# Optimization experiments

Measured on AMD Instinct MI355X. Metric: run time of the kernel, lower is better.

Reference implementation:

```python
import jax, jax.numpy as jnp
import numpy as np

BN_INV = 1.0 / np.float32(np.sqrt(1.0 + 1e-5))  # eval BN with running_mean=0, running_var=1


def _conv(x, w, stride):
    return jax.lax.conv_general_dilated(
        x, w, (stride, stride), [(1, 1), (1, 1)],
        dimension_numbers=('NCHW', 'OIHW', 'NCHW'))


def _se(x, w1, b1, w2, b2):
    # squeeze-excite: global avg pool -> fc -> relu -> fc -> sigmoid -> scale
    y = x.mean(axis=(2, 3))                       # (B, C)
    y = jax.nn.relu(y @ w1.T + b1)
    y = jax.nn.sigmoid(y @ w2.T + b2)
    return x * y[:, :, None, None]


def _squash(s):
    n2 = jnp.sum(s * s, axis=-1, keepdims=True)
    n = jnp.sqrt(n2)
    return s * (n2 / (1.0 + n2)) / (n + 1e-8)


def _block(x, cw, g, b, s1w, s1b, s2w, s2b, stride):
    h = _conv(x, cw, stride)
    h = h * (g * BN_INV)[None, :, None, None] + b[None, :, None, None]
    h = jax.nn.relu(h)
    return _se(h, s1w, s1b, s2w, s2b)


def setup_inputs() -> dict:
    key = jax.random.key(0)
    ks = jax.random.split(key, 32)
    rn = lambda i, shape, s=1.0: s * jax.random.normal(ks[i], shape, dtype=jnp.float32)
    d = {}
    d['x'] = rn(0, (64, 1, 128, 128))
    # feature extractor
    d['conv1_w'] = rn(1, (16, 1, 3, 3), 0.3)
    d['bn1_g'] = 1.0 + rn(2, (16,), 0.1)
    d['bn1_b'] = rn(3, (16,), 0.1)
    d['se1_w1'] = rn(4, (1, 16), 0.2); d['se1_b1'] = rn(5, (1,), 0.1)
    d['se1_w2'] = rn(6, (16, 1), 0.2); d['se1_b2'] = rn(7, (16,), 0.1)
    d['conv2_w'] = rn(8, (32, 16, 3, 3), 0.1)
    d['bn2_g'] = 1.0 + rn(9, (32,), 0.1)
    d['bn2_b'] = rn(10, (32,), 0.1)
    d['se2_w1'] = rn(11, (2, 32), 0.2); d['se2_b1'] = rn(12, (2,), 0.1)
    d['se2_w2'] = rn(13, (32, 2), 0.2); d['se2_b2'] = rn(14, (32,), 0.1)
    d['conv3_w'] = rn(15, (64, 32, 3, 3), 0.07)
    d['bn3_g'] = 1.0 + rn(16, (64,), 0.1)
    d['bn3_b'] = rn(17, (64,), 0.1)
    d['se3_w1'] = rn(18, (4, 64), 0.15); d['se3_b1'] = rn(19, (4,), 0.1)
    d['se3_w2'] = rn(20, (64, 4), 0.15); d['se3_b2'] = rn(21, (64,), 0.1)
    # primary capsules conv: 64 -> 8 caps * 8 dim = 64 channels, stride 2
    d['pc_w'] = rn(22, (64, 64, 3, 3), 0.05)
    d['pc_b'] = rn(23, (64,), 0.05)
    # digit capsule transform: (1, 2048, 3, 16, 8)
    d['W_digit'] = 0.01 * jax.random.normal(ks[24], (1, 2048, 3, 16, 8), dtype=jnp.float32)
    return d


def reference(x, conv1_w, bn1_g, bn1_b, se1_w1, se1_b1, se1_w2, se1_b2,
              conv2_w, bn2_g, bn2_b, se2_w1, se2_b1, se2_w2, se2_b2,
              conv3_w, bn3_g, bn3_b, se3_w1, se3_b1, se3_w2, se3_b2,
              pc_w, pc_b, W_digit):
    h = _block(x, conv1_w, bn1_g, bn1_b, se1_w1, se1_b1, se1_w2, se1_b2, 1)
    h = _block(h, conv2_w, bn2_g, bn2_b, se2_w1, se2_b1, se2_w2, se2_b2, 2)
    h = _block(h, conv3_w, bn3_g, bn3_b, se3_w1, se3_b1, se3_w2, se3_b2, 2)
    # primary capsules: conv -> (B, 8 caps, 8 dim, 16*16) -> (B, 2048, 8)
    u = _conv(h, pc_w, 2) + pc_b[None, :, None, None]     # (B, 64, 16, 16)
    B = u.shape[0]
    u = u.reshape(B, 8, 8, -1).transpose(0, 1, 3, 2).reshape(B, -1, 8)
    u = _squash(u)                                        # (B, 2048, 8)
    # u_hat[b,i,c,d] = sum_e W[0,i,c,d,e] * u[b,i,e]  (avoids torch's W.repeat)
    u_hat = jnp.einsum('icde,bie->bicd', W_digit[0], u)   # (B, 2048, 3, 16)
    b_ij = jnp.zeros((B, u_hat.shape[1], u_hat.shape[2], 1), u_hat.dtype)
    v_j = None
    for _ in range(3):  # fixed routing iterations
        c_ij = jax.nn.softmax(b_ij, axis=2)
        s_j = jnp.sum(c_ij * u_hat, axis=1, keepdims=True)  # (B,1,3,16)
        v_j = _squash(s_j)
        b_ij = b_ij + jnp.sum(u_hat * v_j, axis=-1, keepdims=True)
    v = v_j[:, 0]                                          # (B, 3, 16)
    return jnp.sqrt(jnp.sum(v * v, axis=-1))               # (B, 3) class lengths
```

## Files before the change

kernel.cpp:

```cpp
#include <hip/hip_runtime.h>
#include <math.h>

#define BN_INV_F 0.9999950000374997f

__device__ __forceinline__ void gload_lds4(const float* g, float* l) {
    __builtin_amdgcn_global_load_lds(
        (const __attribute__((address_space(1))) void*)g,
        (__attribute__((address_space(3))) void*)l, 4, 0, 0);
}
__device__ __forceinline__ void gload_lds16(const float* g, float* l) {
    __builtin_amdgcn_global_load_lds(
        (const __attribute__((address_space(1))) void*)g,
        (__attribute__((address_space(3))) void*)l, 16, 0, 0);
}

__global__ __launch_bounds__(256) void wtrans_all_k(
    const float* __restrict__ w1, const float* __restrict__ w2,
    const float* __restrict__ w3, const float* __restrict__ wp,
    float* __restrict__ w1t, float* __restrict__ w2t,
    float* __restrict__ w3t, float* __restrict__ wpt)
{
    int i = blockIdx.x * 256 + threadIdx.x;
    if (i < 144) {
        int co = i % 16, k = i / 16;
        w1t[i] = w1[co * 9 + k];
    } else if (i < 4752) {
        int t = i - 144;
        int co = t % 32, rk = t / 32, cin = rk / 9, k = rk % 9;
        w2t[t] = w2[(co * 16 + cin) * 9 + k];
    } else if (i < 23184) {
        int t = i - 4752;
        int co = t % 64, rk = t / 64, cin = rk / 9, k = rk % 9;
        w3t[t] = w3[(co * 32 + cin) * 9 + k];
    } else if (i < 60048) {
        int t = i - 23184;
        int co = t % 64, rk = t / 64, cin = rk / 9, k = rk % 9;
        wpt[t] = wp[(co * 64 + cin) * 9 + k];
    }
}

template <int CIN, int CINB, int COUT, int COB, int HIN, int HOUT, int STRIDE,
          int TW, int ROWS_T, int PPT, int CB, int NTHREADS,
          bool BN_RELU, bool SE_SUM, int HSE_IN, int KSPLIT>
__device__ __forceinline__ void conv_body(
    const float* __restrict__ in, const float* __restrict__ wt,
    const float* __restrict__ gamma, const float* __restrict__ beta,
    float* __restrict__ out, size_t pstride,
    float* __restrict__ se_sum, const float* __restrict__ se_sums_in,
    const float* __restrict__ se_w1, const float* __restrict__ se_b1,
    const float* __restrict__ se_w2, const float* __restrict__ se_b2,
    float inv_spatial)
{
    constexpr int WIN = HIN, WOUT = HOUT;
    constexpr int TH = ROWS_T * PPT;
    constexpr int IH_T = (TH - 1) * STRIDE + 3;
    constexpr int NW = NTHREADS / 64;
    constexpr int NCHUNK = CINB / CB;
    constexpr int SEGS = (WIN >= 64) ? (WIN / 64) : 1;
    constexpr int PAIRS = (IH_T + 1) / 2;
    constexpr int NG = COUT / COB;
    constexpr int IHW = IH_T * WIN;
    constexpr int CHUNK_BYTES = CB * IHW * 4;
    constexpr bool FAST16 = (CHUNK_BYTES % 1024) == 0;
    constexpr int NISS = CHUNK_BYTES / 1024;
    static_assert(NTHREADS == TW * ROWS_T, "geometry");
    static_assert(TW == WOUT, "tile must span full output width");
    static_assert(CINB % CB == 0, "chunking");
    static_assert(WIN % 64 == 0 || WIN == 32, "stage width");

    const int b = blockIdx.z;
    const int gy = blockIdx.y;
    const int ty = blockIdx.x;
    const int tid = threadIdx.x;
    const int wo = tid % TW;
    const int rg = tid / TW;
    const int g = gy % NG;
    const int kk = gy / NG;
    const int cin0 = kk * CINB;

    __shared__ float in_t[2][CB * IH_T * WIN];
    __shared__ float scl[CIN];
    __shared__ float gl[COB], bl[COB];
    __shared__ float red[NW][COB];
    __shared__ float hid[HSE_IN > 0 ? HSE_IN : 1];

    const float* inb = in + (size_t)b * CIN * HIN * WIN;
    const int gr0 = ty * TH * STRIDE - 1;
    const int wos = wo * STRIDE;
    const int wvid = tid >> 6, lane = tid & 63;
    const bool interior = (gr0 >= 0) && (gr0 + IH_T <= HIN);

    auto stage = [&](int c, int buf) {
        const int cb0 = cin0 + c * CB;
        float* bb = &in_t[buf][0];
        if (FAST16 && interior) {
            for (int i = wvid; i < NISS; i += NW) {
                int fe = i * 256 + lane * 4;
                int ci = fe / IHW;
                int rem = fe - ci * IHW;
                int lr = rem / WIN;
                int lc = rem - lr * WIN;
                const float* gsrc = inb + (size_t)(cb0 + ci) * (HIN * WIN)
                                  + (size_t)(gr0 + lr) * WIN + lc;
                gload_lds16(gsrc, bb + i * 256);
            }
        } else if (WIN >= 64) {
            for (int r = wvid; r < CB * IH_T; r += NW) {
                int ci = r / IH_T, lr = r - ci * IH_T;
                int gr = gr0 + lr;
                float* ldst = bb + (ci * IH_T + lr) * WIN;
                if (gr >= 0 && gr < HIN) {
                    const float* gsrc = inb + (size_t)(cb0 + ci) * HIN * WIN + (size_t)gr * WIN;
#pragma unroll
                    for (int s = 0; s < SEGS; ++s)
                        gload_lds4(gsrc + s * 64 + lane, ldst + s * 64);
                } else {
#pragma unroll
                    for (int s = 0; s < SEGS; ++s) ldst[s * 64 + lane] = 0.0f;
                }
            }
        } else {
            for (int pz = wvid; pz < CB * PAIRS; pz += NW) {
                int ci = pz / PAIRS, q = pz - ci * PAIRS;
                int lr0 = q * 2;
                int nr = (lr0 + 1 < IH_T) ? 2 : 1;
                int grr = gr0 + lr0;
                float* ldst = bb + (ci * IH_T + lr0) * WIN;
                if (nr == 2 && grr >= 0 && grr + 1 < HIN) {
                    const float* gsrc = inb + (size_t)(cb0 + ci) * HIN * WIN + (size_t)grr * WIN + lane;
                    gload_lds4(gsrc, ldst);
                } else {
                    for (int e = lane; e < nr * WIN; e += 64) {
                        int rr = e / WIN, cc = e - rr * WIN;
                        int gr = grr + rr;
                        ldst[e] = (gr >= 0 && gr < HIN)
                            ? inb[(size_t)(cb0 + ci) * HIN * WIN + (size_t)gr * WIN + cc] : 0.0f;
                    }
                }
            }
        }
    };

    stage(0, 0);

    if (HSE_IN > 0) {
        if (tid < HSE_IN) {
            float a = se_b1[tid];
            for (int c = 0; c < CIN; ++c)
                a = fmaf(se_sums_in[b * CIN + c] * inv_spatial, se_w1[tid * CIN + c], a);
            hid[tid] = fmaxf(a, 0.0f);
        }
        __syncthreads();
        if (tid < CIN) {
            float a = se_b2[tid];
            for (int h = 0; h < HSE_IN; ++h)
                a = fmaf(hid[h], se_w2[tid * HSE_IN + h], a);
            scl[tid] = 1.0f / (1.0f + expf(-a));
        }
    } else {
        for (int t = tid; t < CIN; t += NTHREADS) scl[t] = 1.0f;
    }
    if (tid < COB) {
        int co = g * COB + tid;
        if (BN_RELU) {
            gl[tid] = gamma[co] * BN_INV_F;
            bl[tid] = beta[co];
        } else {
            gl[tid] = (kk == 0) ? gamma[co] : 0.0f;
        }
    }

    float acc[PPT][COB];
#pragma unroll
    for (int p = 0; p < PPT; ++p)
#pragma unroll
        for (int co = 0; co < COB; ++co) acc[p][co] = 0.0f;

    int cur = 0;
    for (int c = 0; c < NCHUNK; ++c) {
        asm volatile("s_waitcnt vmcnt(0)" ::: "memory");
        __syncthreads();
        if (c + 1 < NCHUNK) stage(c + 1, cur ^ 1);

        const float* bb = &in_t[cur][0];
#pragma unroll
        for (int ci = 0; ci < CB; ++ci) {
            const int cw = cin0 + c * CB + ci;
            const float sc = scl[cw];
            const float* wtap = wt + (size_t)cw * 9 * COUT + g * COB;
            const float* bb_ci = bb + ci * IH_T * WIN;
#pragma unroll
            for (int kh = 0; kh < 3; ++kh) {
#pragma unroll
                for (int kw = 0; kw < 3; ++kw) {
                    const float* wrow = wtap + (kh * 3 + kw) * COUT;
#pragma unroll
                    for (int p = 0; p < PPT; ++p) {
                        const float* row = bb_ci + ((rg + p * ROWS_T) * STRIDE + kh) * WIN;
                        int wi = wos + kw - 1;
                        float v;
                        if (kw == 0) {
                            v = row[wi < 0 ? 0 : wi];
                            if (wi < 0) v = 0.0f;
                        } else if (STRIDE == 1 && kw == 2) {
                            v = row[wi >= WIN ? WIN - 1 : wi];
                            if (wi >= WIN) v = 0.0f;
                        } else {
                            v = row[wi];
                        }
                        v *= sc;
#pragma unroll
                        for (int co = 0; co < COB; ++co)
                            acc[p][co] = fmaf(wrow[co], v, acc[p][co]);
                    }
                }
            }
        }
        cur ^= 1;
    }

    float tsum[COB];
#pragma unroll
    for (int co = 0; co < COB; ++co) tsum[co] = 0.0f;
    float* ob = out + (size_t)kk * pstride
              + ((size_t)b * COUT + (size_t)g * COB) * HOUT * WOUT;
#pragma unroll
    for (int p = 0; p < PPT; ++p) {
        const int ho = ty * TH + rg + p * ROWS_T;
#pragma unroll
        for (int co = 0; co < COB; ++co) {
            float v;
            if (BN_RELU)
                v = fmaxf(fmaf(acc[p][co], gl[co], bl[co]), 0.0f);
            else
                v = acc[p][co] + gl[co];
            ob[(size_t)co * HOUT * WOUT + ho * WOUT + wo] = v;
            tsum[co] += v;
        }
    }

    if (SE_SUM) {
#pragma unroll
        for (int co = 0; co < COB; ++co) {
            float v = tsum[co];
            for (int off = 32; off; off >>= 1) v += __shfl_down(v, off, 64);
            if (lane == 0) red[wvid][co] = v;
        }
        __syncthreads();
        if (tid < COB) {
            float v = 0.0f;
#pragma unroll
            for (int k = 0; k < NW; ++k) v += red[k][tid];
            atomicAdd(&se_sum[b * COUT + g * COB + tid], v);
        }
    }
}

template <int CIN, int CINB, int COUT, int WCO, int HIN, int HOUT, int STRIDE,
          int TW, int PPT, int CB, int NTHREADS,
          bool BN_RELU, bool SE_SUM, int HSE_IN, int KSPLIT>
__device__ __forceinline__ void conv_ws_body(
    const float* __restrict__ in, const float* __restrict__ wt,
    const float* __restrict__ gamma, const float* __restrict__ beta,
    float* __restrict__ out, size_t pstride,
    float* __restrict__ se_sum, const float* __restrict__ se_sums_in,
    const float* __restrict__ se_w1, const float* __restrict__ se_b1,
    const float* __restrict__ se_w2, const float* __restrict__ se_b2,
    float inv_spatial)
{
    constexpr int WIN = HIN, WOUT = HOUT;
    constexpr int NW = NTHREADS / 64;
    constexpr int WROWS = 64 / TW;
    constexpr int TH = WROWS * PPT;
    constexpr int IH_T = (TH - 1) * STRIDE + 3;
    constexpr int COBT = NW * WCO;
    constexpr int NG = COUT / COBT;
    constexpr int NCHUNK = CINB / CB;
    constexpr int SEGS = WIN / 64;
    constexpr int HALF = WIN / 2;
    static_assert(STRIDE == 2, "wave-split body is stride-2 only");
    static_assert(TW == WOUT, "tile spans full width");
    static_assert(CINB % CB == 0, "chunking");
    static_assert(WIN % 64 == 0, "stage width");
    static_assert(COUT % COBT == 0, "cout split");

    const int b = blockIdx.z;
    const int gy = blockIdx.y;
    const int ty = blockIdx.x;
    const int tid = threadIdx.x;
    const int lane = tid & 63;
    const int wvu = __builtin_amdgcn_readfirstlane(tid >> 6);
    const int wo = lane % TW;
    const int rl = lane / TW;
    const int g = gy % NG;
    const int kk = gy / NG;
    const int cin0 = kk * CINB;

    __shared__ float in_t[2][CB * IH_T * WIN];
    __shared__ float scl[CIN];
    __shared__ float gl[COBT], bl[COBT];
    __shared__ float red[NW][WCO];
    __shared__ float hid[HSE_IN > 0 ? HSE_IN : 1];

    const float* inb = in + (size_t)b * CIN * HIN * WIN;
    const int gr0 = ty * TH * STRIDE - 1;

    auto stage = [&](int c, int buf) {
        const int cb0 = cin0 + c * CB;
        float* bb = &in_t[buf][0];
        for (int r = wvu; r < CB * IH_T; r += NW) {
            int ci = r / IH_T, lr = r - ci * IH_T;
            int gr = gr0 + lr;
            float* ldst = bb + (ci * IH_T + lr) * WIN;
            if (gr >= 0 && gr < HIN) {
                const float* gsrc = inb + (size_t)(cb0 + ci) * HIN * WIN + (size_t)gr * WIN;
#pragma unroll
                for (int s = 0; s < SEGS; ++s) {
                    int p = s * 64 + lane;
                    int half = p / HALF;
                    int idx = p - half * HALF;
                    gload_lds4(gsrc + 2 * idx + half, ldst + s * 64);
                }
            } else {
#pragma unroll
                for (int s = 0; s < SEGS; ++s) ldst[s * 64 + lane] = 0.0f;
            }
        }
    };

    stage(0, 0);

    if (HSE_IN > 0) {
        if (tid < HSE_IN) {
            float a = se_b1[tid];
            for (int c = 0; c < CIN; ++c)
                a = fmaf(se_sums_in[b * CIN + c] * inv_spatial, se_w1[tid * CIN + c], a);
            hid[tid] = fmaxf(a, 0.0f);
        }
        __syncthreads();
        if (tid < CIN) {
            float a = se_b2[tid];
            for (int h = 0; h < HSE_IN; ++h)
                a = fmaf(hid[h], se_w2[tid * HSE_IN + h], a);
            scl[tid] = 1.0f / (1.0f + expf(-a));
        }
    } else {
        for (int t = tid; t < CIN; t += NTHREADS) scl[t] = 1.0f;
    }
    if (tid < COBT) {
        int co = g * COBT + tid;
        if (BN_RELU) {
            gl[tid] = gamma[co] * BN_INV_F;
            bl[tid] = beta[co];
        } else {
            gl[tid] = (kk == 0) ? gamma[co] : 0.0f;
        }
    }

    float acc[PPT][WCO];
#pragma unroll
    for (int p = 0; p < PPT; ++p)
#pragma unroll
        for (int co = 0; co < WCO; ++co) acc[p][co] = 0.0f;

    int cur = 0;
    for (int c = 0; c < NCHUNK; ++c) {
        asm volatile("s_waitcnt vmcnt(0)" ::: "memory");
        __syncthreads();
        if (c + 1 < NCHUNK) stage(c + 1, cur ^ 1);

        const float* bb = &in_t[cur][0];
#pragma unroll
        for (int ci = 0; ci < CB; ++ci) {
            const int cw = cin0 + c * CB + ci;
            const float sc = scl[cw];
            const float* wtap = wt + (size_t)cw * 9 * COUT + g * COBT + wvu * WCO;
            const float* bb_ci = bb + ci * IH_T * WIN;
#pragma unroll
            for (int kh = 0; kh < 3; ++kh) {
                float iwv[PPT][3];
#pragma unroll
                for (int p = 0; p < PPT; ++p) {
                    const float* row = bb_ci + ((rl + p * WROWS) * STRIDE + kh) * WIN;
                    float e  = row[wo];
                    float om = row[HALF + ((wo == 0) ? 0 : wo - 1)];
                    if (wo == 0) om = 0.0f;
                    float op = row[HALF + wo];
                    iwv[p][0] = om * sc;
                    iwv[p][1] = e * sc;
                    iwv[p][2] = op * sc;
                }
#pragma unroll
                for (int kw = 0; kw < 3; ++kw) {
                    const float* wrow = wtap + (kh * 3 + kw) * COUT;
#pragma unroll
                    for (int p = 0; p < PPT; ++p) {
                        const float v = iwv[p][kw];
#pragma unroll
                        for (int co = 0; co < WCO; ++co)
                            acc[p][co] = fmaf(wrow[co], v, acc[p][co]);
                    }
                }
            }
        }
        cur ^= 1;
    }

    float tsum[WCO];
#pragma unroll
    for (int co = 0; co < WCO; ++co) tsum[co] = 0.0f;
    float* ob = out + (size_t)kk * pstride
              + ((size_t)b * COUT + (size_t)g * COBT + (size_t)wvu * WCO) * HOUT * WOUT;
#pragma unroll
    for (int p = 0; p < PPT; ++p) {
        const int ho = ty * TH + rl + p * WROWS;
#pragma unroll
        for (int co = 0; co < WCO; ++co) {
            float v;
            if (BN_RELU)
                v = fmaxf(fmaf(acc[p][co], gl[wvu * WCO + co], bl[wvu * WCO + co]), 0.0f);
            else
                v = acc[p][co] + gl[wvu * WCO + co];
            ob[(size_t)co * HOUT * WOUT + ho * WOUT + wo] = v;
            tsum[co] += v;
        }
    }

    if (SE_SUM) {
#pragma unroll
        for (int co = 0; co < WCO; ++co) {
            float v = tsum[co];
            for (int off = 32; off; off >>= 1) v += __shfl_down(v, off, 64);
            if (lane == 0) red[wvu][co] = v;
        }
        __syncthreads();
        if (lane < WCO)
            atomicAdd(&se_sum[b * COUT + g * COBT + wvu * WCO + lane], red[wvu][lane]);
    }
}

#define CONV_ARGS \
    const float* __restrict__ in, const float* __restrict__ wt, \
    const float* __restrict__ gamma, const float* __restrict__ beta, \
    float* __restrict__ out, size_t pstride, float* __restrict__ se_sum, \
    const float* __restrict__ se_sums_in, \
    const float* __restrict__ se_w1, const float* __restrict__ se_b1, \
    const float* __restrict__ se_w2, const float* __restrict__ se_b2, \
    float inv_spatial
#define CONV_PASS in, wt, gamma, beta, out, pstride, se_sum, se_sums_in, \
    se_w1, se_b1, se_w2, se_b2, inv_spatial

__global__ __launch_bounds__(256) void conv1_k(CONV_ARGS) {
    conv_body<1, 1, 16, 16, 128, 128, 1, 128, 2, 2, 1, 256, true, true, 0, 1>(CONV_PASS);
}
__global__ __launch_bounds__(256) void conv2_k(CONV_ARGS) {
    conv_ws_body<16, 16, 32, 8, 128, 64, 2, 64, 2, 4, 256, true, true, 1, 1>(CONV_PASS);
}
__global__ __launch_bounds__(512) void conv3_k(CONV_ARGS) {
    conv_ws_body<32, 32, 64, 8, 64, 32, 2, 32, 1, 8, 512, true, true, 2, 1>(CONV_PASS);
}
__global__ __launch_bounds__(256) void pc_k(CONV_ARGS) {
    conv_body<64, 16, 64, 16, 32, 16, 2, 16, 16, 1, 4, 256, false, false, 4, 4>(CONV_PASS);
}

__global__ __launch_bounds__(256) void squash_uhat_k(
    const float* __restrict__ up, size_t pstride,
    const float* __restrict__ W, float* __restrict__ u_hat)
{
    const int base = blockIdx.x * 256;
    const int tid = threadIdx.x;
    __shared__ float ush[256][8];

    {
        const int cap = base + tid;
        const int b = cap >> 11, i = cap & 2047;
        const int chi = i >> 8, spx = i & 255;
        const size_t off = ((size_t)(b * 64 + chi * 8)) * 256 + spx;
        float s[8];
        float n2 = 0.0f;
#pragma unroll
        for (int j = 0; j < 8; j++) {
            const size_t o = off + (size_t)j * 256;
            s[j] = (up[o] + up[o + pstride]) + (up[o + 2 * pstride] + up[o + 3 * pstride]);
            n2 = fmaf(s[j], s[j], n2);
        }
        const float n = sqrtf(n2);
        const float f = (n2 / (1.0f + n2)) / (n + 1e-8f);
#pragma unroll
        for (int j = 0; j < 8; j++) ush[tid][j] = s[j] * f;
    }
    __syncthreads();

    float* ob = u_hat + (size_t)base * 48;
#pragma unroll 4
    for (int k = 0; k < 48; ++k) {
        int o = tid + k * 256;
        int c = o / 48, cd = o % 48;
        int gi = (base + c) & 2047;
        const float* wp = W + (size_t)gi * 384 + cd * 8;
        float a = 0.0f;
#pragma unroll
        for (int e = 0; e < 8; e++) a = fmaf(wp[e], ush[c][e], a);
        ob[o] = a;
    }
}

template <int IT>
__global__ __launch_bounds__(256) void sweep_k(const float* __restrict__ u_hat,
                                               const float* __restrict__ s_hist,
                                               float* __restrict__ s_out)
{
    const int b = blockIdx.y;
    const int i = blockIdx.x * 256 + threadIdx.x;
    const int tid = threadIdx.x;
    __shared__ float vsh[IT > 0 ? IT : 1][48];
    __shared__ float fac[IT > 0 ? IT : 1][3];
    __shared__ float red[4][48];

    const float4* qp = (const float4*)(u_hat + ((size_t)b * 2048 + i) * 48);
    float uhv[48];
#pragma unroll
    for (int q = 0; q < 12; ++q) {
        float4 t = qp[q];
        uhv[q * 4 + 0] = t.x; uhv[q * 4 + 1] = t.y;
        uhv[q * 4 + 2] = t.z; uhv[q * 4 + 3] = t.w;
    }

    if (IT > 0) {
        if (tid < IT * 48) {
            int t = tid / 48, c = tid % 48;
            vsh[t][c] = s_hist[((size_t)t * 64 + b) * 48 + c];
        }
        __syncthreads();
        if (tid < IT * 3) {
            int t = tid / 3, j = tid % 3;
            float n2 = 0.0f;
            for (int d = 0; d < 16; ++d) { float s = vsh[t][j * 16 + d]; n2 = fmaf(s, s, n2); }
            float n = sqrtf(n2);
            fac[t][j] = (n2 / (1.0f + n2)) / (n + 1e-8f);
        }
        __syncthreads();
        if (tid < IT * 48) {
            int t = tid / 48, c = tid % 48;
            vsh[t][c] *= fac[t][c / 16];
        }
        __syncthreads();
    }

    float c0, c1, c2;
    if (IT == 0) {
        c0 = c1 = c2 = (1.0f / 3.0f);
    } else {
        float b0 = 0.0f, b1 = 0.0f, b2 = 0.0f;
#pragma unroll
        for (int t = 0; t < IT; ++t)
#pragma unroll
            for (int d = 0; d < 16; ++d) {
                b0 = fmaf(uhv[d],      vsh[t][d],      b0);
                b1 = fmaf(uhv[16 + d], vsh[t][16 + d], b1);
                b2 = fmaf(uhv[32 + d], vsh[t][32 + d], b2);
            }
        float m = fmaxf(b0, fmaxf(b1, b2));
        float e0 = expf(b0 - m), e1 = expf(b1 - m), e2 = expf(b2 - m);
        float inv = 1.0f / (e0 + e1 + e2);
        c0 = e0 * inv; c1 = e1 * inv; c2 = e2 * inv;
    }

    float sp[48];
#pragma unroll
    for (int d = 0; d < 16; ++d) {
        sp[d]      = c0 * uhv[d];
        sp[16 + d] = c1 * uhv[16 + d];
        sp[32 + d] = c2 * uhv[32 + d];
    }
    const int lane = tid & 63, wv = tid >> 6;
#pragma unroll
    for (int j = 0; j < 48; ++j) {
        float x = sp[j];
        for (int off = 32; off; off >>= 1) x += __shfl_down(x, off, 64);
        if (lane == 0) red[wv][j] = x;
    }
    __syncthreads();
    if (tid < 48) {
        float x = red[0][tid] + red[1][tid] + red[2][tid] + red[3][tid];
        atomicAdd(&s_out[(size_t)b * 48 + tid], x);
    }
}

__global__ __launch_bounds__(64) void route_out_k(const float* __restrict__ s2,
                                                  float* __restrict__ out)
{
    const int b = blockIdx.x;
    __shared__ float s[48];
    if (threadIdx.x < 48) s[threadIdx.x] = s2[(size_t)b * 48 + threadIdx.x];
    __syncthreads();
    if (threadIdx.x < 3) {
        int j = threadIdx.x;
        float n2 = 0.0f;
        for (int d = 0; d < 16; ++d) { float v = s[j * 16 + d]; n2 = fmaf(v, v, n2); }
        float n = sqrtf(n2);
        float fc = (n2 / (1.0f + n2)) / (n + 1e-8f);
        out[b * 3 + j] = fc * n;
    }
}

extern "C" void kernel_launch(void* const* d_in, const int* in_sizes, int n_in,
                              void* d_out, int out_size, void* d_ws, size_t ws_size,
                              hipStream_t stream)
{
    const float* x       = (const float*)d_in[0];
    const float* conv1_w = (const float*)d_in[1];
    const float* bn1_g   = (const float*)d_in[2];
    const float* bn1_b   = (const float*)d_in[3];
    const float* se1_w1  = (const float*)d_in[4];
    const float* se1_b1  = (const float*)d_in[5];
    const float* se1_w2  = (const float*)d_in[6];
    const float* se1_b2  = (const float*)d_in[7];
    const float* conv2_w = (const float*)d_in[8];
    const float* bn2_g   = (const float*)d_in[9];
    const float* bn2_b   = (const float*)d_in[10];
    const float* se2_w1  = (const float*)d_in[11];
    const float* se2_b1  = (const float*)d_in[12];
    const float* se2_w2  = (const float*)d_in[13];
    const float* se2_b2  = (const float*)d_in[14];
    const float* conv3_w = (const float*)d_in[15];
    const float* bn3_g   = (const float*)d_in[16];
    const float* bn3_b   = (const float*)d_in[17];
    const float* se3_w1  = (const float*)d_in[18];
    const float* se3_b1  = (const float*)d_in[19];
    const float* se3_w2  = (const float*)d_in[20];
    const float* se3_b2  = (const float*)d_in[21];
    const float* pc_w    = (const float*)d_in[22];
    const float* pc_b    = (const float*)d_in[23];
    const float* W_digit = (const float*)d_in[24];

    float* ws = (float*)d_ws;
    float* h1     = ws;
    float* h2     = ws + 16777216;
    float* h3     = ws;
    float* uparts = ws + 4194304;
    float* u_hat  = ws + 9437184;
    float* sums   = ws + 25165824;
    float* s1 = sums, *s2 = sums + 1024, *s3 = sums + 3072;
    float* s_buf  = sums + 7168;
    float* w1t    = ws + 25182272;
    float* w2t    = w1t + 144;
    float* w3t    = w2t + 4608;
    float* wpt    = w3t + 18432;

    hipMemsetAsync(sums, 0, 16448 * sizeof(float), stream);
    wtrans_all_k<<<235, 256, 0, stream>>>(conv1_w, conv2_w, conv3_w, pc_w,
                                          w1t, w2t, w3t, wpt);

    conv1_k<<<dim3(32, 1, 64), 256, 0, stream>>>(
        x, w1t, bn1_g, bn1_b, h1, 0, s1,
        nullptr, nullptr, nullptr, nullptr, nullptr, 0.0f);

    conv2_k<<<dim3(32, 1, 64), 256, 0, stream>>>(
        h1, w2t, bn2_g, bn2_b, h2, 0, s2,
        s1, se1_w1, se1_b1, se1_w2, se1_b2, 1.0f / 16384.0f);

    conv3_k<<<dim3(16, 1, 64), 512, 0, stream>>>(
        h2, w3t, bn3_g, bn3_b, h3, 0, s3,
        s2, se2_w1, se2_b1, se2_w2, se2_b2, 1.0f / 4096.0f);

    pc_k<<<dim3(1, 16, 64), 256, 0, stream>>>(
        h3, wpt, pc_b, nullptr, uparts, (size_t)1048576, nullptr,
        s3, se3_w1, se3_b1, se3_w2, se3_b2, 1.0f / 1024.0f);

    squash_uhat_k<<<512, 256, 0, stream>>>(uparts, (size_t)1048576, W_digit, u_hat);

    sweep_k<0><<<dim3(8, 64), 256, 0, stream>>>(u_hat, s_buf, s_buf + 0 * 64 * 48);
    sweep_k<1><<<dim3(8, 64), 256, 0, stream>>>(u_hat, s_buf, s_buf + 1 * 64 * 48);
    sweep_k<2><<<dim3(8, 64), 256, 0, stream>>>(u_hat, s_buf, s_buf + 2 * 64 * 48);
    route_out_k<<<64, 64, 0, stream>>>(s_buf + 2 * 64 * 48, (float*)d_out);
}
```

Before: 227.4 us.

## Triple-buffer conv input staging with partial vmcnt waits and retune conv3

Converts the wave-split stride-2 conv body from double to triple LDS buffering, prefetching two chunks ahead. Interior tiles now wait only until the current chunk's DMA has landed (partial vmcnt) rather than draining all loads, with a fast path that skips bounds checks. conv3 is changed to 256 threads with a larger per-wave output-channel count. The extra LDS buffer and the larger per-thread accumulator set may reduce occupancy.

```diff
diff --git a/kernel.cpp b/kernel.cpp
--- a/kernel.cpp
+++ b/kernel.cpp
@@ -278,11 +278,15 @@
     constexpr int NCHUNK = CINB / CB;
     constexpr int SEGS = WIN / 64;
     constexpr int HALF = WIN / 2;
+    constexpr int ROWS = CB * IH_T;
+    constexpr int NPW = (ROWS / NW) * SEGS;
     static_assert(STRIDE == 2, "wave-split body is stride-2 only");
     static_assert(TW == WOUT, "tile spans full width");
     static_assert(CINB % CB == 0, "chunking");
     static_assert(WIN % 64 == 0, "stage width");
     static_assert(COUT % COBT == 0, "cout split");
+    static_assert(ROWS % NW == 0, "uniform DMA count per wave");
+    static_assert(NCHUNK >= 2, "pipeline depth");
 
     const int b = blockIdx.z;
     const int gy = blockIdx.y;
@@ -296,7 +300,7 @@
     const int kk = gy / NG;
     const int cin0 = kk * CINB;
 
-    __shared__ float in_t[2][CB * IH_T * WIN];
+    __shared__ float in_t[3][CB * IH_T * WIN];
     __shared__ float scl[CIN];
     __shared__ float gl[COBT], bl[COBT];
     __shared__ float red[NW][WCO];
@@ -304,16 +308,16 @@
 
     const float* inb = in + (size_t)b * CIN * HIN * WIN;
     const int gr0 = ty * TH * STRIDE - 1;
+    const bool interior = (gr0 >= 0) && (gr0 + IH_T <= HIN);
 
     auto stage = [&](int c, int buf) {
         const int cb0 = cin0 + c * CB;
         float* bb = &in_t[buf][0];
-        for (int r = wvu; r < CB * IH_T; r += NW) {
-            int ci = r / IH_T, lr = r - ci * IH_T;
-            int gr = gr0 + lr;
-            float* ldst = bb + (ci * IH_T + lr) * WIN;
-            if (gr >= 0 && gr < HIN) {
-                const float* gsrc = inb + (size_t)(cb0 + ci) * HIN * WIN + (size_t)gr * WIN;
+        if (interior) {
+            for (int r = wvu; r < ROWS; r += NW) {
+                int ci = r / IH_T, lr = r - ci * IH_T;
+                const float* gsrc = inb + (size_t)(cb0 + ci) * HIN * WIN + (size_t)(gr0 + lr) * WIN;
+                float* ldst = bb + r * WIN;
 #pragma unroll
                 for (int s = 0; s < SEGS; ++s) {
                     int p = s * 64 + lane;
@@ -321,14 +325,28 @@
                     int idx = p - half * HALF;
                     gload_lds4(gsrc + 2 * idx + half, ldst + s * 64);
                 }
-            } else {
-#pragma unroll
-                for (int s = 0; s < SEGS; ++s) ldst[s * 64 + lane] = 0.0f;
             }
+        } else {
+            for (int r = wvu; r < ROWS; r += NW) {
+                int ci = r / IH_T, lr = r - ci * IH_T;
+                int gr = gr0 + lr;
+                float* ldst = bb + r * WIN;
+                if (gr >= 0 && gr < HIN) {
+                    const float* gsrc = inb + (size_t)(cb0 + ci) * HIN * WIN + (size_t)gr * WIN;
+#pragma unroll
+                    for (int s = 0; s < SEGS; ++s) {
+                        int p = s * 64 + lane;
+                        int half = p / HALF;
+                        int idx = p - half * HALF;
+                        gload_lds4(gsrc + 2 * idx + half, ldst + s * 64);
+                    }
+                } else {
+#pragma unroll
+                    for (int s = 0; s < SEGS; ++s) ldst[s * 64 + lane] = 0.0f;
+                }
+            }
         }
     };
-
-    stage(0, 0);
 
     if (HSE_IN > 0) {
         if (tid < HSE_IN) {
@@ -356,6 +374,10 @@
             gl[tid] = (kk == 0) ? gamma[co] : 0.0f;
         }
     }
+    __syncthreads();
+
+    stage(0, 0);
+    stage(1, 1);
 
     float acc[PPT][WCO];
 #pragma unroll
@@ -363,13 +385,20 @@
 #pragma unroll
         for (int co = 0; co < WCO; ++co) acc[p][co] = 0.0f;
 
-    int cur = 0;
     for (int c = 0; c < NCHUNK; ++c) {
-        asm volatile("s_waitcnt vmcnt(0)" ::: "memory");
-        __syncthreads();
-        if (c + 1 < NCHUNK) stage(c + 1, cur ^ 1);
-
-        const float* bb = &in_t[cur][0];
+        if (interior) {
+            if (c + 1 < NCHUNK)
+                asm volatile("s_waitcnt vmcnt(%0)" :: "i"(NPW) : "memory");
+            else
+                asm volatile("s_waitcnt vmcnt(0)" ::: "memory");
+        } else {
+            asm volatile("s_waitcnt vmcnt(0) lgkmcnt(0)" ::: "memory");
+        }
+        __builtin_amdgcn_s_barrier();
+        __builtin_amdgcn_sched_barrier(0);
+        if (c + 2 < NCHUNK) stage(c + 2, (c + 2) % 3);
+
+        const float* bb = &in_t[c % 3][0];
 #pragma unroll
         for (int ci = 0; ci < CB; ++ci) {
             const int cw = cin0 + c * CB + ci;
@@ -403,7 +432,6 @@
                 }
             }
         }
-        cur ^= 1;
     }
 
     float tsum[WCO];
@@ -456,8 +484,8 @@
 __global__ __launch_bounds__(256) void conv2_k(CONV_ARGS) {
     conv_ws_body<16, 16, 32, 8, 128, 64, 2, 64, 2, 4, 256, true, true, 1, 1>(CONV_PASS);
 }
-__global__ __launch_bounds__(512) void conv3_k(CONV_ARGS) {
-    conv_ws_body<32, 32, 64, 8, 64, 32, 2, 32, 1, 8, 512, true, true, 2, 1>(CONV_PASS);
+__global__ __launch_bounds__(256) void conv3_k(CONV_ARGS) {
+    conv_ws_body<32, 32, 64, 16, 64, 32, 2, 32, 1, 8, 256, true, true, 2, 1>(CONV_PASS);
 }
 __global__ __launch_bounds__(256) void pc_k(CONV_ARGS) {
     conv_body<64, 16, 64, 16, 32, 16, 2, 16, 16, 1, 4, 256, false, false, 4, 4>(CONV_PASS);
@@ -660,7 +688,7 @@
         h1, w2t, bn2_g, bn2_b, h2, 0, s2,
         s1, se1_w1, se1_b1, se1_w2, se1_b2, 1.0f / 16384.0f);
 
-    conv3_k<<<dim3(16, 1, 64), 512, 0, stream>>>(
+    conv3_k<<<dim3(16, 1, 64), 256, 0, stream>>>(
         h2, w3t, bn3_g, bn3_b, h3, 0, s3,
         s2, se2_w1, se2_b1, se2_w2, se2_b2, 1.0f / 4096.0f);
 
```

After: 224.6 us. No clear change (-1.3%).
